# Kernel optimization log

Hardware: AMD Instinct MI355X
Metric: run time of the kernel (lower is better)

The kernel has to match this reference:

```python
import jax, jax.numpy as jnp
import numpy as np

N = 100000   # nodes
D = 128      # in_feats
H = 128      # hidden_size
E = 500000   # message edges
EP = 100000  # positive pair edges
EN = 500000  # negative pair edges


def setup_inputs() -> dict:
    key = jax.random.key(0)
    ks = jax.random.split(key, 20)
    s = 1.0 / np.sqrt(H)
    f32 = jnp.float32
    inp = {
        "x": jax.random.normal(ks[0], (N, D), f32),
        "src": jax.random.randint(ks[1], (E,), 0, N, jnp.int32),
        "dst": jax.random.randint(ks[2], (E,), 0, N, jnp.int32),
        "pos_src": jax.random.randint(ks[3], (EP,), 0, N, jnp.int32),
        "pos_dst": jax.random.randint(ks[4], (EP,), 0, N, jnp.int32),
        "neg_src": jax.random.randint(ks[5], (EN,), 0, N, jnp.int32),
        "neg_dst": jax.random.randint(ks[6], (EN,), 0, N, jnp.int32),
        # SAGEConv layer 0 (in->hid) and layer 1 (hid->hid)
        "W_self0": jax.random.normal(ks[7], (D, H), f32) * s,
        "W_neigh0": jax.random.normal(ks[8], (D, H), f32) * s,
        "b0": jnp.zeros((H,), f32),
        "W_self1": jax.random.normal(ks[9], (H, H), f32) * s,
        "W_neigh1": jax.random.normal(ks[10], (H, H), f32) * s,
        "b1": jnp.zeros((H,), f32),
        # EdgeDecoder MLP: hid->hid->hid->1
        "dW1": jax.random.normal(ks[11], (H, H), f32) * s,
        "db1": jnp.zeros((H,), f32),
        "dW2": jax.random.normal(ks[12], (H, H), f32) * s,
        "db2": jnp.zeros((H,), f32),
        "dW3": jax.random.normal(ks[13], (H, 1), f32) * s,
        "db3": jnp.zeros((1,), f32),
    }
    return inp


def _sage_mean(h, src, dst, W_self, W_neigh, b, n_nodes):
    # mean-aggregate neighbor features: gather src feats, segment-sum over dst
    agg = jax.ops.segment_sum(h[src], dst, num_segments=n_nodes)       # [N, d]
    deg = jax.ops.segment_sum(jnp.ones((src.shape[0],), h.dtype), dst,
                              num_segments=n_nodes)                     # [N]
    h_neigh = agg / jnp.maximum(deg, 1.0)[:, None]
    return h @ W_self + h_neigh @ W_neigh + b


def _edge_decode(h, e_src, e_dst, W1, b1, W2, b2, W3, b3):
    z = h[e_src] * h[e_dst]                    # [E_pair, H]
    z = jax.nn.relu(z @ W1 + b1)
    z = jax.nn.relu(z @ W2 + b2)
    return z @ W3 + b3                         # [E_pair, 1]


def reference(x, src, dst, pos_src, pos_dst, neg_src, neg_dst,
              W_self0, W_neigh0, b0, W_self1, W_neigh1, b1,
              dW1, db1, dW2, db2, dW3, db3):
    n = x.shape[0]
    h = jax.nn.relu(_sage_mean(x, src, dst, W_self0, W_neigh0, b0, n))
    h = _sage_mean(h, src, dst, W_self1, W_neigh1, b1, n)  # no act on last layer
    h_pos = _edge_decode(h, pos_src, pos_dst, dW1, db1, dW2, db2, dW3, db3)
    h_neg = _edge_decode(h, neg_src, neg_dst, dW1, db1, dW2, db2, dW3, db3)
    return (h_pos, h_neg)
```

## Files before the change

### kernel.cpp

```cpp
#include <hip/hip_runtime.h>
#include <hip/hip_bf16.h>

#define HD 128

typedef unsigned int u32;
typedef unsigned short u16;
typedef __attribute__((ext_vector_type(8))) short short8;
typedef __attribute__((ext_vector_type(4))) float f32x4;

__device__ __forceinline__ float bf2f(u16 u) {
    return __uint_as_float(((u32)u) << 16);
}
__device__ __forceinline__ u16 f2bf(float f) {
    u32 u = __float_as_uint(f);
    u32 r = (u + 0x7fffu + ((u >> 16) & 1u)) >> 16;
    return (u16)r;
}
__device__ __forceinline__ u32 pk2bf(float lo, float hi) {
    __hip_bfloat162 h = __float22bfloat162_rn(make_float2(lo, hi));
    union { __hip_bfloat162 h; u32 u; } cv; cv.h = h;
    return cv.u;
}
__device__ __forceinline__ float ldf(const void* p, size_t i, bool f32m) {
    return f32m ? ((const float*)p)[i] : bf2f(((const u16*)p)[i]);
}

__global__ void detect_mode(const u32* __restrict__ x, int* __restrict__ mode) {
    __shared__ int cnt_s;
    if (threadIdx.x == 0) cnt_s = 0;
    __syncthreads();
    u32 e = (x[threadIdx.x] >> 23) & 0xFFu;
    if (e >= 90u && e < 170u) atomicAdd(&cnt_s, 1);
    __syncthreads();
    if (threadIdx.x == 0) mode[0] = (cnt_s >= 128) ? 1 : 0;
}

__global__ void pack_w6(const void* __restrict__ W0, const void* __restrict__ W1,
                        const void* __restrict__ W2, const void* __restrict__ W3,
                        const void* __restrict__ W4, const void* __restrict__ W5,
                        u16* __restrict__ out, const int* __restrict__ gmode) {
    const bool f32m = gmode[0] != 0;
    int gid = blockIdx.x * 256 + threadIdx.x;
    if (gid >= 6 * 16384) return;
    int sel = gid >> 14, idx = gid & 16383;
    const void* W = sel == 0 ? W0 : sel == 1 ? W1 : sel == 2 ? W2 :
                    sel == 3 ? W3 : sel == 4 ? W4 : W5;
    int j = idx & 7, lane = (idx >> 3) & 63, ks = (idx >> 9) & 3, nt = idx >> 11;
    int k = ks * 32 + (lane >> 4) * 8 + j;
    int n = nt * 16 + (lane & 15);
    out[gid] = f2bf(ldf(W, (size_t)k * HD + n, f32m));
}

__global__ void cnt_count(const int* __restrict__ dst, int* __restrict__ cnt, int e) {
    int i = blockIdx.x * 256 + threadIdx.x;
    if (i < e) atomicAdd(&cnt[dst[i]], 1);
}

__global__ void scan_blocks(const int* __restrict__ cnt, int* __restrict__ rowptr,
                            int* __restrict__ bsum, int n) {
    __shared__ int s[256];
    int t = threadIdx.x, gid = blockIdx.x * 256 + t;
    int v = (gid < n) ? cnt[gid] : 0;
    s[t] = v; __syncthreads();
    #pragma unroll
    for (int off = 1; off < 256; off <<= 1) {
        int x = (t >= off) ? s[t - off] : 0;
        __syncthreads();
        s[t] += x;
        __syncthreads();
    }
    if (gid < n) rowptr[gid] = s[t] - v;
    if (t == 255) bsum[blockIdx.x] = s[255];
}

__global__ void scan_bsum(int* __restrict__ bsum, int nb) {
    __shared__ int s[1024];
    __shared__ int carry;
    int t = threadIdx.x;
    if (t == 0) carry = 0;
    __syncthreads();
    for (int base = 0; base < nb; base += 1024) {
        int i = base + t;
        int v = (i < nb) ? bsum[i] : 0;
        s[t] = v; __syncthreads();
        #pragma unroll
        for (int off = 1; off < 1024; off <<= 1) {
            int x = (t >= off) ? s[t - off] : 0;
            __syncthreads();
            s[t] += x;
            __syncthreads();
        }
        if (i < nb) bsum[i] = carry + s[t] - v;
        __syncthreads();
        if (t == 0) carry += s[1023];
        __syncthreads();
    }
}

__global__ void scan_add(int* __restrict__ rowptr, const int* __restrict__ bsum,
                         int n, int e) {
    int gid = blockIdx.x * 256 + threadIdx.x;
    if (gid < n) rowptr[gid] += bsum[blockIdx.x];
    else if (gid == n) rowptr[n] = e;
}

__global__ void csr_fill(const int* __restrict__ src, const int* __restrict__ dst,
                         const int* __restrict__ rowptr, int* __restrict__ cur,
                         int* __restrict__ cidx, int e) {
    int i = blockIdx.x * 256 + threadIdx.x;
    if (i >= e) return;
    int d = dst[i];
    int p = rowptr[d] + atomicAdd(&cur[d], 1);
    cidx[p] = src[i];
}

__global__ __launch_bounds__(256) void agg_gather(
    const void* __restrict__ h, const int* __restrict__ rowptr,
    const int* __restrict__ cidx, u16* __restrict__ aggb,
    const int* __restrict__ gmode, int use_mode, int n) {
    const bool f32m = use_mode && (gmode[0] != 0);
    int wid = (blockIdx.x * 256 + threadIdx.x) >> 6;
    int lane = threadIdx.x & 63;
    if (wid >= n) return;
    int s0 = rowptr[wid], s1 = rowptr[wid + 1];
    float a0 = 0.f, a1 = 0.f;
    int i = s0;
    for (; i + 1 < s1; i += 2) {
        int sA = cidx[i], sB = cidx[i + 1];
        if (f32m) {
            float2 vA = *(const float2*)((const float*)h + (size_t)sA * HD + lane * 2);
            float2 vB = *(const float2*)((const float*)h + (size_t)sB * HD + lane * 2);
            a0 += vA.x + vB.x; a1 += vA.y + vB.y;
        } else {
            u32 vA = *(const u32*)((const u16*)h + (size_t)sA * HD + lane * 2);
            u32 vB = *(const u32*)((const u16*)h + (size_t)sB * HD + lane * 2);
            a0 += __uint_as_float(vA << 16) + __uint_as_float(vB << 16);
            a1 += __uint_as_float(vA & 0xffff0000u) + __uint_as_float(vB & 0xffff0000u);
        }
    }
    if (i < s1) {
        int sA = cidx[i];
        if (f32m) {
            float2 vA = *(const float2*)((const float*)h + (size_t)sA * HD + lane * 2);
            a0 += vA.x; a1 += vA.y;
        } else {
            u32 vA = *(const u32*)((const u16*)h + (size_t)sA * HD + lane * 2);
            a0 += __uint_as_float(vA << 16);
            a1 += __uint_as_float(vA & 0xffff0000u);
        }
    }
    float iv = 1.f / fmaxf((float)(s1 - s0), 1.f);
    *(u32*)&aggb[(size_t)wid * HD + lane * 2] = pk2bf(a0 * iv, a1 * iv);
}

template <bool RELU>
__global__ __launch_bounds__(256) void sage_mfma(
    const void* __restrict__ X, const u16* __restrict__ aggb,
    const u16* __restrict__ Wsp, const u16* __restrict__ Wnp,
    const void* __restrict__ bias, u16* __restrict__ hout,
    const int* __restrict__ gmode, int use_mode, int n) {
    __shared__ u16 zS[64 * 136];
    __shared__ u16 zN[64 * 136];
    u16* outh = zS;

    const bool f32m = gmode[0] != 0;
    const bool inf32 = use_mode && f32m;
    const int t = threadIdx.x;
    const int n0 = blockIdx.x * 64;
    const int lane = t & 63;
    const int w = t >> 6;
    const int cl = lane & 15, quad = lane >> 4;

    #pragma unroll
    for (int i = 0; i < 8; i++) {
        int idx = t + i * 256;
        int e = idx >> 5, fg = (idx & 31) * 4;
        int node = n0 + e;
        u32 p0 = 0, p1 = 0, q0 = 0, q1 = 0;
        if (node < n) {
            if (inf32) {
                float4 v = *(const float4*)((const float*)X + (size_t)node * HD + fg);
                p0 = pk2bf(v.x, v.y); p1 = pk2bf(v.z, v.w);
            } else {
                uint2 v = *(const uint2*)((const u16*)X + (size_t)node * HD + fg);
                p0 = v.x; p1 = v.y;
            }
            uint2 a = *(const uint2*)&aggb[(size_t)node * HD + fg];
            q0 = a.x; q1 = a.y;
        }
        *(uint2*)&zS[e * 136 + fg] = make_uint2(p0, p1);
        *(uint2*)&zN[e * 136 + fg] = make_uint2(q0, q1);
    }
    __syncthreads();

    f32x4 acc[2][4];
    #pragma unroll
    for (int ft = 0; ft < 2; ft++) {
        int f0 = w * 32 + ft * 16 + quad * 4;
        f32x4 bv;
        bv[0] = ldf(bias, f0 + 0, f32m);
        bv[1] = ldf(bias, f0 + 1, f32m);
        bv[2] = ldf(bias, f0 + 2, f32m);
        bv[3] = ldf(bias, f0 + 3, f32m);
        #pragma unroll
        for (int et = 0; et < 4; et++) acc[ft][et] = bv;
    }
    #pragma unroll
    for (int ks = 0; ks < 4; ks++) {
        short8 aS[2], aN[2], bS[4], bN[4];
        #pragma unroll
        for (int ft = 0; ft < 2; ft++) {
            aS[ft] = ((const short8*)Wsp)[((w * 2 + ft) * 4 + ks) * 64 + lane];
            aN[ft] = ((const short8*)Wnp)[((w * 2 + ft) * 4 + ks) * 64 + lane];
        }
        #pragma unroll
        for (int et = 0; et < 4; et++) {
            bS[et] = *(const short8*)&zS[(et * 16 + cl) * 136 + ks * 32 + quad * 8];
            bN[et] = *(const short8*)&zN[(et * 16 + cl) * 136 + ks * 32 + quad * 8];
        }
        #pragma unroll
        for (int ft = 0; ft < 2; ft++)
            #pragma unroll
            for (int et = 0; et < 4; et++) {
                acc[ft][et] = __builtin_amdgcn_mfma_f32_16x16x32_bf16(
                    aS[ft], bS[et], acc[ft][et], 0, 0, 0);
                acc[ft][et] = __builtin_amdgcn_mfma_f32_16x16x32_bf16(
                    aN[ft], bN[et], acc[ft][et], 0, 0, 0);
            }
    }
    __syncthreads();

    #pragma unroll
    for (int ft = 0; ft < 2; ft++) {
        int f0 = w * 32 + ft * 16 + quad * 4;
        #pragma unroll
        for (int et = 0; et < 4; et++) {
            f32x4 v = acc[ft][et];
            float v0 = RELU ? fmaxf(v[0], 0.f) : v[0];
            float v1 = RELU ? fmaxf(v[1], 0.f) : v[1];
            float v2 = RELU ? fmaxf(v[2], 0.f) : v[2];
            float v3 = RELU ? fmaxf(v[3], 0.f) : v[3];
            *(uint2*)&outh[(et * 16 + cl) * 136 + f0] =
                make_uint2(pk2bf(v0, v1), pk2bf(v2, v3));
        }
    }
    __syncthreads();
    #pragma unroll
    for (int i = 0; i < 8; i++) {
        int idx = t + i * 256;
        int e = idx >> 5, fg = (idx & 31) * 4;
        int node = n0 + e;
        if (node < n)
            *(uint2*)&hout[(size_t)node * HD + fg] = *(const uint2*)&outh[e * 136 + fg];
    }
}

__device__ __forceinline__ void gemm128(
    const u16* zin, u16* zout, const u16* __restrict__ Wp,
    const void* __restrict__ bias, bool f32m, int w, int lane) {
    const int cl = lane & 15, quad = lane >> 4;
    f32x4 acc[2][4];
    #pragma unroll
    for (int ft = 0; ft < 2; ft++) {
        int f0 = w * 32 + ft * 16 + quad * 4;
        f32x4 bv;
        bv[0] = ldf(bias, f0 + 0, f32m);
        bv[1] = ldf(bias, f0 + 1, f32m);
        bv[2] = ldf(bias, f0 + 2, f32m);
        bv[3] = ldf(bias, f0 + 3, f32m);
        #pragma unroll
        for (int et = 0; et < 4; et++) acc[ft][et] = bv;
    }
    #pragma unroll
    for (int ks = 0; ks < 4; ks++) {
        short8 a[2], b[4];
        #pragma unroll
        for (int ft = 0; ft < 2; ft++)
            a[ft] = ((const short8*)Wp)[((w * 2 + ft) * 4 + ks) * 64 + lane];
        #pragma unroll
        for (int et = 0; et < 4; et++)
            b[et] = *(const short8*)&zin[(et * 16 + cl) * 136 + ks * 32 + quad * 8];
        #pragma unroll
        for (int ft = 0; ft < 2; ft++)
            #pragma unroll
            for (int et = 0; et < 4; et++)
                acc[ft][et] = __builtin_amdgcn_mfma_f32_16x16x32_bf16(
                    a[ft], b[et], acc[ft][et], 0, 0, 0);
    }
    #pragma unroll
    for (int ft = 0; ft < 2; ft++) {
        int f0 = w * 32 + ft * 16 + quad * 4;
        #pragma unroll
        for (int et = 0; et < 4; et++) {
            f32x4 v = acc[ft][et];
            *(uint2*)&zout[(et * 16 + cl) * 136 + f0] = make_uint2(
                pk2bf(fmaxf(v[0], 0.f), fmaxf(v[1], 0.f)),
                pk2bf(fmaxf(v[2], 0.f), fmaxf(v[3], 0.f)));
        }
    }
}

__global__ __launch_bounds__(256) void edge_decode_mfma(
    const u16* __restrict__ h,
    const int* __restrict__ psrc, const int* __restrict__ pdst, int ep, int PB,
    const int* __restrict__ nsrc, const int* __restrict__ ndst, int en,
    const u16* __restrict__ W1p, const void* __restrict__ b1,
    const u16* __restrict__ W2p, const void* __restrict__ b2,
    const void* __restrict__ W3, const void* __restrict__ b3,
    void* __restrict__ out, const int* __restrict__ gmode) {
    __shared__ u16 zA[64 * 136];
    __shared__ u16 zB[64 * 136];
    __shared__ float w3f[HD];
    __shared__ float psum[256];
    const bool f32m = gmode[0] != 0;
    const int t = threadIdx.x;
    const int b = blockIdx.x;
    const int* esrc; const int* edst; int e0, obase, ne;
    if (b < PB) { esrc = psrc; edst = pdst; e0 = b * 64;        obase = 0;  ne = ep; }
    else        { esrc = nsrc; edst = ndst; e0 = (b - PB) * 64; obase = ep; ne = en; }
    const int lane = t & 63;
    const int w = t >> 6;

    if (t < HD) w3f[t] = ldf(W3, t, f32m);

    #pragma unroll
    for (int i = 0; i < 8; i++) {
        int idx = t + i * 256;
        int e = idx >> 5, fg = (idx & 31) * 4;
        int eg = e0 + e;
        u32 p0 = 0, p1 = 0;
        if (eg < ne) {
            int s = esrc[eg], d = edst[eg];
            uint2 a = *(const uint2*)(h + (size_t)s * HD + fg);
            uint2 b2v = *(const uint2*)(h + (size_t)d * HD + fg);
            float x0 = __uint_as_float(a.x << 16)         * __uint_as_float(b2v.x << 16);
            float x1 = __uint_as_float(a.x & 0xffff0000u) * __uint_as_float(b2v.x & 0xffff0000u);
            float x2 = __uint_as_float(a.y << 16)         * __uint_as_float(b2v.y << 16);
            float x3 = __uint_as_float(a.y & 0xffff0000u) * __uint_as_float(b2v.y & 0xffff0000u);
            p0 = pk2bf(x0, x1);
            p1 = pk2bf(x2, x3);
        }
        *(uint2*)&zA[e * 136 + fg] = make_uint2(p0, p1);
    }
    __syncthreads();

    gemm128(zA, zB, W1p, b1, f32m, w, lane);
    __syncthreads();
    gemm128(zB, zA, W2p, b2, f32m, w, lane);
    __syncthreads();

    {
        int e = t & 63, kc = t >> 6;
        float s = 0.f;
        #pragma unroll 8
        for (int k = kc * 32; k < kc * 32 + 32; k++)
            s = fmaf(bf2f(zA[e * 136 + k]), w3f[k], s);
        psum[t] = s;
    }
    __syncthreads();
    if (t < 64) {
        int eg = e0 + t;
        if (eg < ne) {
            float sum = ldf(b3, 0, f32m) + psum[t] + psum[t + 64] + psum[t + 128] + psum[t + 192];
            if (f32m) ((float*)out)[obase + eg] = sum;
            else      ((u16*)out)[obase + eg]   = f2bf(sum);
        }
    }
}

extern "C" void kernel_launch(void* const* d_in, const int* in_sizes, int n_in,
                              void* d_out, int out_size, void* d_ws, size_t ws_size,
                              hipStream_t stream) {
    const void* x      = d_in[0];
    const int* src     = (const int*)d_in[1];
    const int* dst     = (const int*)d_in[2];
    const int* pos_src = (const int*)d_in[3];
    const int* pos_dst = (const int*)d_in[4];
    const int* neg_src = (const int*)d_in[5];
    const int* neg_dst = (const int*)d_in[6];
    const void* Ws0 = d_in[7];
    const void* Wn0 = d_in[8];
    const void* b0  = d_in[9];
    const void* Ws1 = d_in[10];
    const void* Wn1 = d_in[11];
    const void* b1  = d_in[12];
    const void* dW1 = d_in[13];
    const void* db1 = d_in[14];
    const void* dW2 = d_in[15];
    const void* db2 = d_in[16];
    const void* dW3 = d_in[17];
    const void* db3 = d_in[18];

    const int n  = in_sizes[0] / HD;
    const int e  = in_sizes[1];
    const int ep = in_sizes[3];
    const int en = in_sizes[5];
    const int NB = (n + 255) / 256;
    const int PB = (ep + 63) / 64, NDB = (en + 63) / 64;

    char* base = (char*)d_ws;
    u16* aggb = (u16*)d_ws;
    u16* h1   = aggb + (size_t)n * HD;
    size_t off = (size_t)n * HD * 4;
    int* mode = (int*)(base + off);      off += 16;
    int* rowptr = (int*)(base + off);    off += (size_t)(n + 1) * 4; off = (off + 15) & ~(size_t)15;
    int* cnt = (int*)(base + off);       off += (size_t)n * 4;       off = (off + 15) & ~(size_t)15;
    int* cidx = (int*)(base + off);      off += (size_t)e * 4;       off = (off + 15) & ~(size_t)15;
    int* bsum = (int*)(base + off);      off += (size_t)NB * 4;      off = (off + 15) & ~(size_t)15;
    u16* Wpk  = (u16*)(base + off);
    u16* W1p  = Wpk;
    u16* W2p  = Wpk + 16384;
    u16* Ws0p = Wpk + 2 * 16384;
    u16* Wn0p = Wpk + 3 * 16384;
    u16* Ws1p = Wpk + 4 * 16384;
    u16* Wn1p = Wpk + 5 * 16384;

    detect_mode<<<dim3(1), dim3(256), 0, stream>>>((const u32*)x, mode);

    hipMemsetAsync(cnt, 0, (size_t)n * 4, stream);
    cnt_count<<<dim3((e + 255) / 256), dim3(256), 0, stream>>>(dst, cnt, e);
    scan_blocks<<<dim3(NB), dim3(256), 0, stream>>>(cnt, rowptr, bsum, n);
    scan_bsum<<<dim3(1), dim3(1024), 0, stream>>>(bsum, NB);
    scan_add<<<dim3((n + 256) / 256), dim3(256), 0, stream>>>(rowptr, bsum, n, e);
    hipMemsetAsync(cnt, 0, (size_t)n * 4, stream);
    csr_fill<<<dim3((e + 255) / 256), dim3(256), 0, stream>>>(src, dst, rowptr, cnt, cidx, e);

    pack_w6<<<dim3(384), dim3(256), 0, stream>>>(dW1, dW2, Ws0, Wn0, Ws1, Wn1, Wpk, mode);

    agg_gather<<<dim3((n * 64 + 255) / 256), dim3(256), 0, stream>>>(
        x, rowptr, cidx, aggb, mode, 1, n);
    sage_mfma<true><<<dim3((n + 63) / 64), dim3(256), 0, stream>>>(
        x, aggb, Ws0p, Wn0p, b0, h1, mode, 1, n);

    agg_gather<<<dim3((n * 64 + 255) / 256), dim3(256), 0, stream>>>(
        h1, rowptr, cidx, aggb, mode, 0, n);
    sage_mfma<false><<<dim3((n + 63) / 64), dim3(256), 0, stream>>>(
        h1, aggb, Ws1p, Wn1p, b1, aggb , mode, 0, n);

    edge_decode_mfma<<<dim3(PB + NDB), dim3(256), 0, stream>>>(
        aggb, pos_src, pos_dst, ep, PB, neg_src, neg_dst, en,
        W1p, db1, W2p, db2, dW3, db3, d_out, mode);
}
```

Measured before the change: 427.6 us.

## Swizzle LDS tiles, fuse final decoder layer into registers, unroll gather by four

```diff
diff --git a/kernel.cpp b/kernel.cpp
--- a/kernel.cpp
+++ b/kernel.cpp
@@ -23,6 +23,9 @@
 }
 __device__ __forceinline__ float ldf(const void* p, size_t i, bool f32m) {
     return f32m ? ((const float*)p)[i] : bf2f(((const u16*)p)[i]);
+}
+__device__ __forceinline__ int swz(int row, int col) {
+    return row * 128 + ((((col >> 3) ^ (row & 7)) << 3) | (col & 7));
 }
 
 __global__ void detect_mode(const u32* __restrict__ x, int* __restrict__ mode) {
@@ -125,28 +128,36 @@
     int s0 = rowptr[wid], s1 = rowptr[wid + 1];
     float a0 = 0.f, a1 = 0.f;
     int i = s0;
-    for (; i + 1 < s1; i += 2) {
-        int sA = cidx[i], sB = cidx[i + 1];
-        if (f32m) {
+    if (f32m) {
+        for (; i + 3 < s1; i += 4) {
+            int sA = cidx[i], sB = cidx[i + 1], sC = cidx[i + 2], sD = cidx[i + 3];
             float2 vA = *(const float2*)((const float*)h + (size_t)sA * HD + lane * 2);
             float2 vB = *(const float2*)((const float*)h + (size_t)sB * HD + lane * 2);
-            a0 += vA.x + vB.x; a1 += vA.y + vB.y;
-        } else {
+            float2 vC = *(const float2*)((const float*)h + (size_t)sC * HD + lane * 2);
+            float2 vD = *(const float2*)((const float*)h + (size_t)sD * HD + lane * 2);
+            a0 += (vA.x + vB.x) + (vC.x + vD.x);
+            a1 += (vA.y + vB.y) + (vC.y + vD.y);
+        }
+        for (; i < s1; i++) {
+            float2 v = *(const float2*)((const float*)h + (size_t)cidx[i] * HD + lane * 2);
+            a0 += v.x; a1 += v.y;
+        }
+    } else {
+        for (; i + 3 < s1; i += 4) {
+            int sA = cidx[i], sB = cidx[i + 1], sC = cidx[i + 2], sD = cidx[i + 3];
             u32 vA = *(const u32*)((const u16*)h + (size_t)sA * HD + lane * 2);
             u32 vB = *(const u32*)((const u16*)h + (size_t)sB * HD + lane * 2);
-            a0 += __uint_as_float(vA << 16) + __uint_as_float(vB << 16);
-            a1 += __uint_as_float(vA & 0xffff0000u) + __uint_as_float(vB & 0xffff0000u);
-        }
-    }
-    if (i < s1) {
-        int sA = cidx[i];
-        if (f32m) {
-            float2 vA = *(const float2*)((const float*)h + (size_t)sA * HD + lane * 2);
-            a0 += vA.x; a1 += vA.y;
-        } else {
-            u32 vA = *(const u32*)((const u16*)h + (size_t)sA * HD + lane * 2);
-            a0 += __uint_as_float(vA << 16);
-            a1 += __uint_as_float(vA & 0xffff0000u);
+            u32 vC = *(const u32*)((const u16*)h + (size_t)sC * HD + lane * 2);
+            u32 vD = *(const u32*)((const u16*)h + (size_t)sD * HD + lane * 2);
+            a0 += (__uint_as_float(vA << 16) + __uint_as_float(vB << 16))
+                + (__uint_as_float(vC << 16) + __uint_as_float(vD << 16));
+            a1 += (__uint_as_float(vA & 0xffff0000u) + __uint_as_float(vB & 0xffff0000u))
+                + (__uint_as_float(vC & 0xffff0000u) + __uint_as_float(vD & 0xffff0000u));
+        }
+        for (; i < s1; i++) {
+            u32 v = *(const u32*)((const u16*)h + (size_t)cidx[i] * HD + lane * 2);
+            a0 += __uint_as_float(v << 16);
+            a1 += __uint_as_float(v & 0xffff0000u);
         }
     }
     float iv = 1.f / fmaxf((float)(s1 - s0), 1.f);
@@ -159,8 +170,8 @@
     const u16* __restrict__ Wsp, const u16* __restrict__ Wnp,
     const void* __restrict__ bias, u16* __restrict__ hout,
     const int* __restrict__ gmode, int use_mode, int n) {
-    __shared__ u16 zS[64 * 136];
-    __shared__ u16 zN[64 * 136];
+    __shared__ u16 zS[64 * 128];
+    __shared__ u16 zN[64 * 128];
     u16* outh = zS;
 
     const bool f32m = gmode[0] != 0;
@@ -188,8 +199,9 @@
             uint2 a = *(const uint2*)&aggb[(size_t)node * HD + fg];
             q0 = a.x; q1 = a.y;
         }
-        *(uint2*)&zS[e * 136 + fg] = make_uint2(p0, p1);
-        *(uint2*)&zN[e * 136 + fg] = make_uint2(q0, q1);
+        int sa = swz(e, fg);
+        *(uint2*)&zS[sa] = make_uint2(p0, p1);
+        *(uint2*)&zN[sa] = make_uint2(q0, q1);
     }
     __syncthreads();
 
@@ -215,8 +227,9 @@
         }
         #pragma unroll
         for (int et = 0; et < 4; et++) {
-            bS[et] = *(const short8*)&zS[(et * 16 + cl) * 136 + ks * 32 + quad * 8];
-            bN[et] = *(const short8*)&zN[(et * 16 + cl) * 136 + ks * 32 + quad * 8];
+            int sa = swz(et * 16 + cl, ks * 32 + quad * 8);
+            bS[et] = *(const short8*)&zS[sa];
+            bN[et] = *(const short8*)&zN[sa];
         }
         #pragma unroll
         for (int ft = 0; ft < 2; ft++)
@@ -240,7 +253,7 @@
             float v1 = RELU ? fmaxf(v[1], 0.f) : v[1];
             float v2 = RELU ? fmaxf(v[2], 0.f) : v[2];
             float v3 = RELU ? fmaxf(v[3], 0.f) : v[3];
-            *(uint2*)&outh[(et * 16 + cl) * 136 + f0] =
+            *(uint2*)&outh[swz(et * 16 + cl, f0)] =
                 make_uint2(pk2bf(v0, v1), pk2bf(v2, v3));
         }
     }
@@ -251,7 +264,7 @@
         int e = idx >> 5, fg = (idx & 31) * 4;
         int node = n0 + e;
         if (node < n)
-            *(uint2*)&hout[(size_t)node * HD + fg] = *(const uint2*)&outh[e * 136 + fg];
+            *(uint2*)&hout[(size_t)node * HD + fg] = *(const uint2*)&outh[swz(e, fg)];
     }
 }
 
@@ -279,7 +292,7 @@
             a[ft] = ((const short8*)Wp)[((w * 2 + ft) * 4 + ks) * 64 + lane];
         #pragma unroll
         for (int et = 0; et < 4; et++)
-            b[et] = *(const short8*)&zin[(et * 16 + cl) * 136 + ks * 32 + quad * 8];
+            b[et] = *(const short8*)&zin[swz(et * 16 + cl, ks * 32 + quad * 8)];
         #pragma unroll
         for (int ft = 0; ft < 2; ft++)
             #pragma unroll
@@ -293,7 +306,7 @@
         #pragma unroll
         for (int et = 0; et < 4; et++) {
             f32x4 v = acc[ft][et];
-            *(uint2*)&zout[(et * 16 + cl) * 136 + f0] = make_uint2(
+            *(uint2*)&zout[swz(et * 16 + cl, f0)] = make_uint2(
                 pk2bf(fmaxf(v[0], 0.f), fmaxf(v[1], 0.f)),
                 pk2bf(fmaxf(v[2], 0.f), fmaxf(v[3], 0.f)));
         }
@@ -308,9 +321,8 @@
     const u16* __restrict__ W2p, const void* __restrict__ b2,
     const void* __restrict__ W3, const void* __restrict__ b3,
     void* __restrict__ out, const int* __restrict__ gmode) {
-    __shared__ u16 zA[64 * 136];
-    __shared__ u16 zB[64 * 136];
-    __shared__ float w3f[HD];
+    __shared__ u16 zA[64 * 128];
+    __shared__ u16 zB[64 * 128];
     __shared__ float psum[256];
     const bool f32m = gmode[0] != 0;
     const int t = threadIdx.x;
@@ -320,8 +332,7 @@
     else        { esrc = nsrc; edst = ndst; e0 = (b - PB) * 64; obase = ep; ne = en; }
     const int lane = t & 63;
     const int w = t >> 6;
-
-    if (t < HD) w3f[t] = ldf(W3, t, f32m);
+    const int cl = lane & 15, quad = lane >> 4;
 
     #pragma unroll
     for (int i = 0; i < 8; i++) {
@@ -340,28 +351,74 @@
             p0 = pk2bf(x0, x1);
             p1 = pk2bf(x2, x3);
         }
-        *(uint2*)&zA[e * 136 + fg] = make_uint2(p0, p1);
+        *(uint2*)&zA[swz(e, fg)] = make_uint2(p0, p1);
     }
     __syncthreads();
 
     gemm128(zA, zB, W1p, b1, f32m, w, lane);
     __syncthreads();
-    gemm128(zB, zA, W2p, b2, f32m, w, lane);
-    __syncthreads();
-
-    {
-        int e = t & 63, kc = t >> 6;
-        float s = 0.f;
-        #pragma unroll 8
-        for (int k = kc * 32; k < kc * 32 + 32; k++)
-            s = fmaf(bf2f(zA[e * 136 + k]), w3f[k], s);
-        psum[t] = s;
+
+    f32x4 acc[2][4];
+    #pragma unroll
+    for (int ft = 0; ft < 2; ft++) {
+        int f0 = w * 32 + ft * 16 + quad * 4;
+        f32x4 bv;
+        bv[0] = ldf(b2, f0 + 0, f32m);
+        bv[1] = ldf(b2, f0 + 1, f32m);
+        bv[2] = ldf(b2, f0 + 2, f32m);
+        bv[3] = ldf(b2, f0 + 3, f32m);
+        #pragma unroll
+        for (int et = 0; et < 4; et++) acc[ft][et] = bv;
+    }
+    #pragma unroll
+    for (int ks = 0; ks < 4; ks++) {
+        short8 a[2], bb[4];
+        #pragma unroll
+        for (int ft = 0; ft < 2; ft++)
+            a[ft] = ((const short8*)W2p)[((w * 2 + ft) * 4 + ks) * 64 + lane];
+        #pragma unroll
+        for (int et = 0; et < 4; et++)
+            bb[et] = *(const short8*)&zB[swz(et * 16 + cl, ks * 32 + quad * 8)];
+        #pragma unroll
+        for (int ft = 0; ft < 2; ft++)
+            #pragma unroll
+            for (int et = 0; et < 4; et++)
+                acc[ft][et] = __builtin_amdgcn_mfma_f32_16x16x32_bf16(
+                    a[ft], bb[et], acc[ft][et], 0, 0, 0);
+    }
+    float p[4] = {0.f, 0.f, 0.f, 0.f};
+    #pragma unroll
+    for (int ft = 0; ft < 2; ft++) {
+        int f0 = w * 32 + ft * 16 + quad * 4;
+        float w3v0 = ldf(W3, f0 + 0, f32m);
+        float w3v1 = ldf(W3, f0 + 1, f32m);
+        float w3v2 = ldf(W3, f0 + 2, f32m);
+        float w3v3 = ldf(W3, f0 + 3, f32m);
+        #pragma unroll
+        for (int et = 0; et < 4; et++) {
+            f32x4 v = acc[ft][et];
+            p[et] = fmaf(fmaxf(v[0], 0.f), w3v0, p[et]);
+            p[et] = fmaf(fmaxf(v[1], 0.f), w3v1, p[et]);
+            p[et] = fmaf(fmaxf(v[2], 0.f), w3v2, p[et]);
+            p[et] = fmaf(fmaxf(v[3], 0.f), w3v3, p[et]);
+        }
+    }
+    #pragma unroll
+    for (int et = 0; et < 4; et++) {
+        p[et] += __shfl_xor(p[et], 16);
+        p[et] += __shfl_xor(p[et], 32);
+    }
+    if (lane < 16) {
+        #pragma unroll
+        for (int et = 0; et < 4; et++)
+            psum[w * 64 + et * 16 + lane] = p[et];
     }
     __syncthreads();
     if (t < 64) {
         int eg = e0 + t;
         if (eg < ne) {
-            float sum = ldf(b3, 0, f32m) + psum[t] + psum[t + 64] + psum[t + 128] + psum[t + 192];
+            float sum = ldf(b3, 0, f32m) + (psum[t] + psum[64 + t])
+                      + (psum[128 + t] + psum[192 + t]);
             if (f32m) ((float*)out)[obase + eg] = sum;
             else      ((u16*)out)[obase + eg]   = f2bf(sum);
         }
```

After: 438.2 us. 1.02x slower.
